# Performance work log

Measured on AMD Instinct MI355X. Metric: run time of the kernel, lower is better.

The kernel has to match this reference:

```python
import jax, jax.numpy as jnp
import numpy as np

B, T, HID = 1, 256, 2048
H, D = 16, 128
KD = H * D
CONV = 4
MAX_CG = 30
LAMB_LB = 0.25
NORM_EPS = 1e-5


def setup_inputs() -> dict:
    key = jax.random.key(0)
    ks = jax.random.split(key, 10)
    s = 0.02
    init_lamb = float(np.log(np.exp(1.0 - LAMB_LB) - 1.0))  # softplus^-1(1 - lower_bound)
    return {
        "hidden_states": jax.random.normal(ks[0], (B, T, HID), jnp.float32),
        "Wq": jax.random.normal(ks[1], (HID, KD), jnp.float32) * s,
        "Wk": jax.random.normal(ks[2], (HID, KD), jnp.float32) * s,
        "Wv": jax.random.normal(ks[3], (HID, KD), jnp.float32) * s,
        "Wa": jax.random.normal(ks[4], (HID, H), jnp.float32) * s,
        "ba": jnp.full((H,), 2.0, jnp.float32),
        "Wb": jax.random.normal(ks[5], (HID, H), jnp.float32) * s,
        "bb": jnp.zeros((H,), jnp.float32),
        "conv_wq": jax.random.normal(ks[6], (KD, CONV), jnp.float32) * s,
        "conv_wk": jax.random.normal(ks[7], (KD, CONV), jnp.float32) * s,
        "lambda_params": jnp.full((KD,), init_lamb, jnp.float32),
        "o_norm_w": jnp.ones((D,), jnp.float32),
        "Wo": jax.random.normal(ks[8], (KD, HID), jnp.float32) * s,
    }


def short_conv_silu(x, w):
    # depthwise causal conv over time; x [b,t,c], w [c,k]
    k = w.shape[1]
    xp = jnp.pad(x, ((0, 0), (k - 1, 0), (0, 0)))
    t = x.shape[1]
    y = xp[:, 0:t, :] * w[:, 0]
    for i in range(1, k):
        y = y + xp[:, i:i + t, :] * w[:, i]
    return jax.nn.silu(y)


def l2norm(x):
    return x * jax.lax.rsqrt(jnp.sum(x * x, -1, keepdims=True) + 1e-6)


def rmsnorm(x, w):
    return x * jax.lax.rsqrt(jnp.mean(x * x, -1, keepdims=True) + NORM_EPS) * w


def cg_solve(A, b):
    # solve A x = b per (batch, head) with fixed CG iterations, x0 = 0
    matvec = lambda p: jnp.einsum('bhij,bhj->bhi', A, p)
    x0 = jnp.zeros_like(b)
    rs0 = jnp.sum(b * b, -1)

    def body(i, st):
        xc, r, p, rs = st
        Ap = matvec(p)
        alpha = rs / (jnp.sum(p * Ap, -1) + 1e-12)
        xc = xc + alpha[..., None] * p
        r = r - alpha[..., None] * Ap
        rs_n = jnp.sum(r * r, -1)
        p = r + (rs_n / (rs + 1e-12))[..., None] * p
        return xc, r, p, rs_n

    xf, _, _, _ = jax.lax.fori_loop(0, MAX_CG, body, (x0, b, b, rs0))
    return xf


def mesa_recurrence(q, k, v, g, beta, lamb_diag):
    # q,k,v [b,t,h,d]; g,beta [b,t,h]; lamb_diag [h,d,d]
    def step(carry, inp):
        h_kk, h_kv = carry
        qt, kt, vt, gt, bt = inp
        decay = jnp.exp(gt)[..., None, None]
        b_ = bt[..., None, None]
        h_kk = h_kk * decay + b_ * (kt[..., :, None] * kt[..., None, :])
        h_kv = h_kv * decay + b_ * (kt[..., :, None] * vt[..., None, :])
        A = h_kk + lamb_diag[None]
        q_star = cg_solve(A, qt)
        ot = jnp.einsum('bhk,bhkv->bhv', q_star, h_kv)
        return (h_kk, h_kv), ot

    init = (jnp.zeros((B, H, D, D), q.dtype), jnp.zeros((B, H, D, D), q.dtype))
    xs = (q.transpose(1, 0, 2, 3), k.transpose(1, 0, 2, 3), v.transpose(1, 0, 2, 3),
          g.transpose(1, 0, 2), beta.transpose(1, 0, 2))
    _, o = jax.lax.scan(step, init, xs)
    return o.transpose(1, 0, 2, 3)  # [b,t,h,d]


def reference(hidden_states, Wq, Wk, Wv, Wa, ba, Wb, bb, conv_wq, conv_wk,
              lambda_params, o_norm_w, Wo):
    x = hidden_states
    q = short_conv_silu(x @ Wq, conv_wq)
    k = short_conv_silu(x @ Wk, conv_wk)
    v = x @ Wv
    q = l2norm(q.reshape(B, T, H, D))
    k = l2norm(k.reshape(B, T, H, D))
    v = v.reshape(B, T, H, D)
    beta = jax.nn.sigmoid(x @ Wb + bb)          # [b,t,h]
    g = jax.nn.log_sigmoid(x @ Wa + ba)          # [b,t,h]
    lamb = (jax.nn.softplus(lambda_params) + LAMB_LB).reshape(H, D)
    lamb_diag = lamb[:, :, None] * jnp.eye(D, dtype=lamb.dtype)  # [h,d,d]
    o = mesa_recurrence(q, k, v, g, beta, lamb_diag)
    o = rmsnorm(o, o_norm_w)
    o = o.reshape(B, T, KD) @ Wo
    return o
```

## Files before the change

kernel.cpp:

```cpp
#include <hip/hip_runtime.h>
#include <math.h>

#define TT 256
#define HIDDEN 2048
#define NH 16
#define HD 128
#define KDIM 2048
#define NCG 30

typedef _Float16 h2 __attribute__((ext_vector_type(2)));
typedef _Float16 h4 __attribute__((ext_vector_type(4)));
typedef _Float16 half8 __attribute__((ext_vector_type(8)));
typedef float floatx4 __attribute__((ext_vector_type(4)));

__device__ __forceinline__ float wave_sum64(float v) {
#pragma unroll
    for (int off = 32; off > 0; off >>= 1) v += __shfl_xor(v, off, 64);
    return v;
}

__device__ __forceinline__ half8 cvt8(const float4 x, const float4 y) {
    half8 f;
    f[0] = (_Float16)x.x; f[1] = (_Float16)x.y; f[2] = (_Float16)x.z; f[3] = (_Float16)x.w;
    f[4] = (_Float16)y.x; f[5] = (_Float16)y.y; f[6] = (_Float16)y.z; f[7] = (_Float16)y.w;
    return f;
}

__device__ __forceinline__ void glds16(const void* g, void* l) {
    __builtin_amdgcn_global_load_lds(
        (const __attribute__((address_space(1))) void*)g,
        (__attribute__((address_space(3))) void*)l, 16, 0, 0);
}

__global__ __launch_bounds__(256) void wtrans_kernel(
    const float* __restrict__ W0, const float* __restrict__ W1,
    const float* __restrict__ W2, const float* __restrict__ W3,
    _Float16* __restrict__ T0, _Float16* __restrict__ T1,
    _Float16* __restrict__ T2, _Float16* __restrict__ T3,
    const float* __restrict__ Wa, const float* __restrict__ Wb,
    _Float16* __restrict__ Tabb)
{
    __shared__ float tile[64][68];
    const int z = blockIdx.z;
    const int tid = threadIdx.x;
    int k0, n0;
    _Float16* __restrict__ T;

    if (z == 4) {
        const int y = blockIdx.y;
        if (y >= 2) return;
        k0 = blockIdx.x * 64; n0 = y * 64;
        T = Tabb;
#pragma unroll
        for (int p = 0; p < 4; p++) {
            const int idx = p * 256 + tid;
            const int r = idx >> 4, c = (idx & 15) * 4;
            float4 v = make_float4(0.f, 0.f, 0.f, 0.f);
            if (y == 0 && c < 32) {
                const float* src = (c < 16) ? &Wa[(size_t)(k0 + r) * NH + c]
                                            : &Wb[(size_t)(k0 + r) * NH + (c - 16)];
                v = *(const float4*)src;
            }
            tile[r][c] = v.x; tile[r][c + 1] = v.y; tile[r][c + 2] = v.z; tile[r][c + 3] = v.w;
        }
    } else {
        const float* __restrict__ W = (z == 0) ? W0 : (z == 1) ? W1 : (z == 2) ? W2 : W3;
        T = (z == 0) ? T0 : (z == 1) ? T1 : (z == 2) ? T2 : T3;
        k0 = blockIdx.x * 64; n0 = blockIdx.y * 64;
#pragma unroll
        for (int p = 0; p < 4; p++) {
            const int idx = p * 256 + tid;
            const int r = idx >> 4, c = (idx & 15) * 4;
            const float4 v = *(const float4*)&W[(size_t)(k0 + r) * KDIM + n0 + c];
            tile[r][c] = v.x; tile[r][c + 1] = v.y; tile[r][c + 2] = v.z; tile[r][c + 3] = v.w;
        }
    }
    __syncthreads();
#pragma unroll
    for (int p = 0; p < 2; p++) {
        const int slot = p * 256 + tid;
        const int ktc = slot >> 6, nn_loc = slot & 63;
        const int gk = k0 + ktc * 8, gn = n0 + nn_loc;
        const int nt = gn >> 7, nn = gn & 127;
        const int kt = gk >> 5, kc = (gk >> 3) & 3;
        half8 o;
#pragma unroll
        for (int j = 0; j < 8; j++) o[j] = (_Float16)tile[ktc * 8 + j][nn_loc];
        *(half8*)&T[(size_t)(((nt * 64 + kt) * 4 + kc)) * 1024 + nn * 8] = o;
    }
}

#define ASTR 72
__global__ __launch_bounds__(256) void gemm_kernel(
    const float* __restrict__ A,
    const _Float16* __restrict__ Bb0, const _Float16* __restrict__ Bb1,
    const _Float16* __restrict__ Bb2, const _Float16* __restrict__ Bb3,
    float* __restrict__ C0, float* __restrict__ C1, float* __restrict__ C2,
    const float* __restrict__ ba, const float* __restrict__ bb,
    float* __restrict__ g, float* __restrict__ beta)
{
    __shared__ __align__(16) _Float16 Bsh[2][8192];
    __shared__ __align__(16) _Float16 Ash[2][32 * ASTR];

    const int tid = threadIdx.x, lane = tid & 63, w = tid >> 6;
    const int q = lane >> 4, l16 = lane & 15;

    const int b = blockIdx.x;
    const int xcd = b & 7, gslot = b >> 3;
    int nt, mt;
    if (gslot < 48) { nt = xcd * 6 + (gslot >> 3); mt = gslot & 7; }
    else           { nt = 48;                      mt = xcd; }
    const int mat = nt >> 4;
    const int ntile = nt & 15;
    const int n0 = ntile * 128;
    const _Float16* __restrict__ Bb = (mat == 0) ? Bb0 : (mat == 1) ? Bb1 : (mat == 2) ? Bb2 : Bb3;
    float* __restrict__ C = (mat == 0) ? C0 : (mat == 1) ? C1 : C2;
    const int m0 = mt * 32;

    const _Float16* __restrict__ Btile = Bb + (size_t)ntile * 262144;
    const int ar = tid >> 3, ac = (tid & 7) * 8;
    const float* __restrict__ Ap = &A[(size_t)(m0 + ar) * KDIM + ac];

    floatx4 acc[2][2] = {};
    float4 ax, ay;

#pragma unroll
    for (int i = 0; i < 4; i++)
        glds16(Btile + (size_t)((w * 4 + i) * 64 + lane) * 8, &Bsh[0][(w * 4 + i) * 512]);
    ax = *(const float4*)&Ap[0]; ay = *(const float4*)&Ap[4];
    *(half8*)&Ash[0][ar * ASTR + ac] = cvt8(ax, ay);
    ax = *(const float4*)&Ap[64]; ay = *(const float4*)&Ap[68];
    __syncthreads();

    const int NSTEP = KDIM / 64;
    for (int s = 0; s < NSTEP; s++) {
        const int cur = s & 1;
        if (s + 1 < NSTEP) {
            const _Float16* src = Btile + (size_t)(s + 1) * 8192;
#pragma unroll
            for (int i = 0; i < 4; i++)
                glds16(src + (size_t)((w * 4 + i) * 64 + lane) * 8, &Bsh[cur ^ 1][(w * 4 + i) * 512]);
        }
#pragma unroll
        for (int kk = 0; kk < 2; kk++) {
            const half8 bf0 = *(const half8*)&Bsh[cur][kk * 4096 + q * 1024 + (w * 32 + l16) * 8];
            const half8 bf1 = *(const half8*)&Bsh[cur][kk * 4096 + q * 1024 + (w * 32 + 16 + l16) * 8];
            const half8 af0 = *(const half8*)&Ash[cur][l16 * ASTR + kk * 32 + q * 8];
            const half8 af1 = *(const half8*)&Ash[cur][(16 + l16) * ASTR + kk * 32 + q * 8];
            acc[0][0] = __builtin_amdgcn_mfma_f32_16x16x32_f16(af0, bf0, acc[0][0], 0, 0, 0);
            acc[0][1] = __builtin_amdgcn_mfma_f32_16x16x32_f16(af0, bf1, acc[0][1], 0, 0, 0);
            acc[1][0] = __builtin_amdgcn_mfma_f32_16x16x32_f16(af1, bf0, acc[1][0], 0, 0, 0);
            acc[1][1] = __builtin_amdgcn_mfma_f32_16x16x32_f16(af1, bf1, acc[1][1], 0, 0, 0);
        }
        if (s + 1 < NSTEP) {
            *(half8*)&Ash[cur ^ 1][ar * ASTR + ac] = cvt8(ax, ay);
            if (s + 2 < NSTEP) {
                ax = *(const float4*)&Ap[(s + 2) * 64];
                ay = *(const float4*)&Ap[(s + 2) * 64 + 4];
            }
        }
        __syncthreads();
    }

    if (mat == 3) {
        if (w == 0) {
            const float bav = ba[l16], bbv = bb[l16];
#pragma unroll
            for (int r = 0; r < 4; r++) {
                const int t0r = m0 + q * 4 + r, t1r = m0 + 16 + q * 4 + r;
                float z0 = acc[0][0][r] + bav;
                g[t0r * NH + l16] = fminf(z0, 0.f) - log1pf(__expf(-fabsf(z0)));
                float z1 = acc[0][1][r] + bbv;
                beta[t0r * NH + l16] = 1.f / (1.f + __expf(-z1));
                float z2 = acc[1][0][r] + bav;
                g[t1r * NH + l16] = fminf(z2, 0.f) - log1pf(__expf(-fabsf(z2)));
                float z3 = acc[1][1][r] + bbv;
                beta[t1r * NH + l16] = 1.f / (1.f + __expf(-z3));
            }
        }
        return;
    }

#pragma unroll
    for (int r = 0; r < 4; r++) {
        C[(size_t)(m0 + q * 4 + r) * KDIM + n0 + w * 32 + l16] = acc[0][0][r];
        C[(size_t)(m0 + q * 4 + r) * KDIM + n0 + w * 32 + 16 + l16] = acc[0][1][r];
        C[(size_t)(m0 + 16 + q * 4 + r) * KDIM + n0 + w * 32 + l16] = acc[1][0][r];
        C[(size_t)(m0 + 16 + q * 4 + r) * KDIM + n0 + w * 32 + 16 + l16] = acc[1][1][r];
    }
}

__global__ __launch_bounds__(256) void gemm64_kernel(
    const float* __restrict__ A, const _Float16* __restrict__ Bb,
    float* __restrict__ C)
{
    __shared__ __align__(16) _Float16 Bsh[2][4096];
    __shared__ __align__(16) _Float16 Ash[2][32 * ASTR];

    const int tid = threadIdx.x, lane = tid & 63, w = tid >> 6;
    const int q = lane >> 4, l16 = lane & 15;
    const int b = blockIdx.x;
    const int xcd = b & 7, gslot = b >> 3;
    const int nt = xcd * 4 + (gslot >> 3), mt = gslot & 7;
    const int n0 = nt * 64, m0 = mt * 32;
    const int nt128 = nt >> 1;
    const size_t nnoff = (size_t)(nt & 1) * 512;

    const _Float16* __restrict__ Btile = Bb + (size_t)nt128 * 262144;
    const int ar = tid >> 3, ac = (tid & 7) * 8;
    const float* __restrict__ Ap = &A[(size_t)(m0 + ar) * KDIM + ac];

    floatx4 acc0 = {}, acc1 = {};
    float4 ax, ay;

    const int c0 = w * 2, c1 = w * 2 + 1;
    auto bsrc = [&](int s, int chunk) {
        const int kt2 = chunk >> 2, kc = chunk & 3;
        return Btile + (size_t)((s * 2 + kt2) * 4 + kc) * 1024 + nnoff + (size_t)lane * 8;
    };

    glds16(bsrc(0, c0), &Bsh[0][c0 * 512]);
    glds16(bsrc(0, c1), &Bsh[0][c1 * 512]);
    ax = *(const float4*)&Ap[0]; ay = *(const float4*)&Ap[4];
    *(half8*)&Ash[0][ar * ASTR + ac] = cvt8(ax, ay);
    ax = *(const float4*)&Ap[64]; ay = *(const float4*)&Ap[68];
    __syncthreads();

    const int NSTEP = KDIM / 64;
    for (int s = 0; s < NSTEP; s++) {
        const int cur = s & 1;
        if (s + 1 < NSTEP) {
            glds16(bsrc(s + 1, c0), &Bsh[cur ^ 1][c0 * 512]);
            glds16(bsrc(s + 1, c1), &Bsh[cur ^ 1][c1 * 512]);
        }
#pragma unroll
        for (int kk = 0; kk < 2; kk++) {
            const half8 bf  = *(const half8*)&Bsh[cur][kk * 2048 + q * 512 + (w * 16 + l16) * 8];
            const half8 af0 = *(const half8*)&Ash[cur][l16 * ASTR + kk * 32 + q * 8];
            const half8 af1 = *(const half8*)&Ash[cur][(16 + l16) * ASTR + kk * 32 + q * 8];
            acc0 = __builtin_amdgcn_mfma_f32_16x16x32_f16(af0, bf, acc0, 0, 0, 0);
            acc1 = __builtin_amdgcn_mfma_f32_16x16x32_f16(af1, bf, acc1, 0, 0, 0);
        }
        if (s + 1 < NSTEP) {
            *(half8*)&Ash[cur ^ 1][ar * ASTR + ac] = cvt8(ax, ay);
            if (s + 2 < NSTEP) {
                ax = *(const float4*)&Ap[(s + 2) * 64];
                ay = *(const float4*)&Ap[(s + 2) * 64 + 4];
            }
        }
        __syncthreads();
    }

#pragma unroll
    for (int r = 0; r < 4; r++) {
        C[(size_t)(m0 + q * 4 + r) * KDIM + n0 + w * 16 + l16] = acc0[r];
        C[(size_t)(m0 + 16 + q * 4 + r) * KDIM + n0 + w * 16 + l16] = acc1[r];
    }
}

__global__ __launch_bounds__(256) void conv_silu_l2_kernel(
    const float* __restrict__ q_pre, const float* __restrict__ k_pre,
    const float* __restrict__ cwq, const float* __restrict__ cwk,
    float* __restrict__ qn, float* __restrict__ kn)
{
    const int t = blockIdx.x, h = blockIdx.y;
    const int which = threadIdx.x >> 7, d = threadIdx.x & 127;
    const int w = threadIdx.x >> 6;
    const int c = h * HD + d;
    const float* pre = which ? k_pre : q_pre;
    const float* cw  = which ? cwk : cwq;
    float y = 0.f;
#pragma unroll
    for (int i = 0; i < 4; i++) {
        const int ts = t - 3 + i;
        if (ts >= 0) y = fmaf(pre[ts * KDIM + c], cw[c * 4 + i], y);
    }
    const float s = y / (1.f + __expf(-y));
    float v = s * s;
#pragma unroll
    for (int off = 32; off > 0; off >>= 1) v += __shfl_down(v, off, 64);
    __shared__ float red[4];
    if ((threadIdx.x & 63) == 0) red[w] = v;
    __syncthreads();
    const float sum = red[which * 2] + red[which * 2 + 1];
    float* dst = which ? kn : qn;
    dst[t * KDIM + c] = s * rsqrtf(sum + 1e-6f);
}

#define PSTR 136
#define YSTR 264

template<int SMAX>
__device__ __forceinline__ void mesa_cg(
    const float* __restrict__ qn, const float* __restrict__ kn, const float* __restrict__ vv,
    const float* __restrict__ g, const float* __restrict__ bet, const float* __restrict__ lp,
    const float* __restrict__ onw, float* __restrict__ out,
    int h, int t0, _Float16* Psh, _Float16* Ysh, float* red,
    float* Gsh, float* bets)
{
    constexpr int NSUB1 = SMAX / 64;
    constexpr int NK2   = SMAX / 32;

    const int tid = threadIdx.x, lane = tid & 63, w = tid >> 6;
    const int quad = lane >> 4, l16 = lane & 15;
    const int tmy = t0 + l16;
    const int dbase = w * 32;

    {
        float sc = g[tid * NH + h];
#pragma unroll
        for (int off = 1; off < 64; off <<= 1) {
            const float o = __shfl_up(sc, off, 64);
            if (lane >= off) sc += o;
        }
        if (lane == 63) red[w] = sc;
        bets[tid] = bet[tid * NH + h];
        __syncthreads();
        float woff = 0.f;
        for (int u = 0; u < w; u++) woff += red[u];
        Gsh[tid] = sc + woff;
        __syncthreads();
    }

    half8 K1[NSUB1][4];
#pragma unroll
    for (int ii = 0; ii < NSUB1; ii++) {
        const int srow = 16 * (w + 4 * ii) + l16;
        const float* kp = &kn[(srow * NH + h) * HD];
#pragma unroll
        for (int kk = 0; kk < 4; kk++) {
            const float4 a = *(const float4*)&kp[kk * 32 + quad * 8];
            const float4 b = *(const float4*)&kp[kk * 32 + quad * 8 + 4];
            K1[ii][kk] = cvt8(a, b);
        }
    }

    half8 KtF[2][NK2];
#pragma unroll
    for (int ss = 0; ss < 2; ss++) {
        const int d = dbase + ss * 16 + l16;
#pragma unroll
        for (int kk = 0; kk < NK2; kk++) {
#pragma unroll
            for (int j = 0; j < 8; j++) {
                const int s = kk * 32 + quad * 8 + j;
                KtF[ss][kk][j] = (_Float16)kn[(s * NH + h) * HD + d];
            }
        }
    }

    half8 Vf[NK2][2];
#pragma unroll
    for (int kk = 0; kk < NK2; kk++) {
#pragma unroll
        for (int ss = 0; ss < 2; ss++) {
            const int dv = dbase + ss * 16 + l16;
#pragma unroll
            for (int j = 0; j < 8; j++) {
                const int s = kk * 32 + quad * 8 + j;
                Vf[kk][ss][j] = (_Float16)vv[(s * NH + h) * HD + dv];
            }
        }
    }

    const float Gt = Gsh[tmy];
    float Wm[NSUB1][4];
#pragma unroll
    for (int ii = 0; ii < NSUB1; ii++)
#pragma unroll
        for (int r = 0; r < 4; r++) {
            const int s = 16 * (w + 4 * ii) + quad * 4 + r;
            Wm[ii][r] = (s <= tmy) ? bets[s] * __expf(Gt - Gsh[s]) : 0.f;
        }
    float lam[8], xv[8], rv[8], pv[8];
#pragma unroll
    for (int ss = 0; ss < 2; ss++)
#pragma unroll
        for (int r = 0; r < 4; r++) {
            const int e = ss * 4 + r;
            const int d = dbase + ss * 16 + quad * 4 + r;
            const float lx = lp[h * HD + d];
            lam[e] = fmaxf(lx, 0.f) + log1pf(__expf(-fabsf(lx))) + 0.25f;
            const float b = qn[(tmy * NH + h) * HD + d];
            xv[e] = 0.f; rv[e] = b; pv[e] = b;
        }
    float rs = 0.f;
#pragma unroll
    for (int e = 0; e < 8; e++) rs += rv[e] * rv[e];
    rs += __shfl_xor(rs, 16, 64); rs += __shfl_xor(rs, 32, 64);

    auto writeP = [&](const float* src) {
#pragma unroll
        for (int ss = 0; ss < 2; ss++) {
            h4 ph;
            ph.x = (_Float16)src[ss * 4 + 0]; ph.y = (_Float16)src[ss * 4 + 1];
            ph.z = (_Float16)src[ss * 4 + 2]; ph.w = (_Float16)src[ss * 4 + 3];
            *(h4*)&Psh[l16 * PSTR + dbase + ss * 16 + quad * 4] = ph;
        }
    };
    writeP(pv);

    for (int it = 0; it <= NCG; it++) {
        __syncthreads();
        floatx4 acc1a[NSUB1] = {}, acc1b[NSUB1] = {};
#pragma unroll
        for (int kk = 0; kk < 2; kk++) {
            const half8 bfa = *(const half8*)&Psh[l16 * PSTR + kk * 32 + quad * 8];
            const half8 bfb = *(const half8*)&Psh[l16 * PSTR + (kk + 2) * 32 + quad * 8];
#pragma unroll
            for (int ii = 0; ii < NSUB1; ii++) {
                acc1a[ii] = __builtin_amdgcn_mfma_f32_16x16x32_f16(K1[ii][kk], bfa, acc1a[ii], 0, 0, 0);
                acc1b[ii] = __builtin_amdgcn_mfma_f32_16x16x32_f16(K1[ii][kk + 2], bfb, acc1b[ii], 0, 0, 0);
            }
        }
#pragma unroll
        for (int ii = 0; ii < NSUB1; ii++) {
            h4 yh;
            yh.x = (_Float16)(Wm[ii][0] * (acc1a[ii][0] + acc1b[ii][0]));
            yh.y = (_Float16)(Wm[ii][1] * (acc1a[ii][1] + acc1b[ii][1]));
            yh.z = (_Float16)(Wm[ii][2] * (acc1a[ii][2] + acc1b[ii][2]));
            yh.w = (_Float16)(Wm[ii][3] * (acc1a[ii][3] + acc1b[ii][3]));
            *(h4*)&Ysh[l16 * YSTR + 16 * (w + 4 * ii) + quad * 4] = yh;
        }
        __syncthreads();
        if (it == NCG) break;

        floatx4 acc2a[2] = {}, acc2b[2] = {};
#pragma unroll
        for (int kk = 0; kk < NK2; kk += 2) {
            const half8 bf0 = *(const half8*)&Ysh[l16 * YSTR + kk * 32 + quad * 8];
            const half8 bf1 = *(const half8*)&Ysh[l16 * YSTR + (kk + 1) * 32 + quad * 8];
#pragma unroll
            for (int ss = 0; ss < 2; ss++) {
                acc2a[ss] = __builtin_amdgcn_mfma_f32_16x16x32_f16(KtF[ss][kk], bf0, acc2a[ss], 0, 0, 0);
                acc2b[ss] = __builtin_amdgcn_mfma_f32_16x16x32_f16(KtF[ss][kk + 1], bf1, acc2b[ss], 0, 0, 0);
            }
        }
        float Ap[8], pAp = 0.f;
#pragma unroll
        for (int ss = 0; ss < 2; ss++)
#pragma unroll
            for (int r = 0; r < 4; r++) {
                const int e = ss * 4 + r;
                Ap[e] = (acc2a[ss][r] + acc2b[ss][r]) + lam[e] * pv[e];
                pAp = fmaf(pv[e], Ap[e], pAp);
            }
        pAp += __shfl_xor(pAp, 16, 64); pAp += __shfl_xor(pAp, 32, 64);
        const float alpha = rs / (pAp + 1e-12f);
        float rsn = 0.f;
#pragma unroll
        for (int e = 0; e < 8; e++) {
            xv[e] = fmaf(alpha, pv[e], xv[e]);
            rv[e] = fmaf(-alpha, Ap[e], rv[e]);
            rsn = fmaf(rv[e], rv[e], rsn);
        }
        rsn += __shfl_xor(rsn, 16, 64); rsn += __shfl_xor(rsn, 32, 64);
        const float bcg = rsn / (rs + 1e-12f);
#pragma unroll
        for (int e = 0; e < 8; e++) pv[e] = fmaf(bcg, pv[e], rv[e]);
        rs = rsn;
        writeP(it == NCG - 1 ? xv : pv);
    }

    floatx4 accOa[2] = {}, accOb[2] = {};
#pragma unroll
    for (int kk = 0; kk < NK2; kk += 2) {
        const half8 af0 = *(const half8*)&Ysh[l16 * YSTR + kk * 32 + quad * 8];
        const half8 af1 = *(const half8*)&Ysh[l16 * YSTR + (kk + 1) * 32 + quad * 8];
#pragma unroll
        for (int ss = 0; ss < 2; ss++) {
            accOa[ss] = __builtin_amdgcn_mfma_f32_16x16x32_f16(af0, Vf[kk][ss], accOa[ss], 0, 0, 0);
            accOb[ss] = __builtin_amdgcn_mfma_f32_16x16x32_f16(af1, Vf[kk + 1][ss], accOb[ss], 0, 0, 0);
        }
    }
    float accO[2][4];
#pragma unroll
    for (int ss = 0; ss < 2; ss++)
#pragma unroll
        for (int r = 0; r < 4; r++) accO[ss][r] = accOa[ss][r] + accOb[ss][r];

    float part[4];
#pragma unroll
    for (int r = 0; r < 4; r++) {
        part[r] = accO[0][r] * accO[0][r] + accO[1][r] * accO[1][r];
#pragma unroll
        for (int off = 1; off < 16; off <<= 1) part[r] += __shfl_xor(part[r], off, 64);
    }
    if (l16 == 0) {
#pragma unroll
        for (int r = 0; r < 4; r++) red[w * 16 + quad * 4 + r] = part[r];
    }
    __syncthreads();
    const float w0 = onw[dbase + l16], w1 = onw[dbase + 16 + l16];
#pragma unroll
    for (int r = 0; r < 4; r++) {
        const int qr = quad * 4 + r;
        const float sumd = red[qr] + red[16 + qr] + red[32 + qr] + red[48 + qr];
        const float sc = rsqrtf(sumd * (1.f / HD) + 1e-5f);
        const int trow = ((t0 + qr) * NH + h) * HD;
        out[trow + dbase + l16] = accO[0][r] * sc * w0;
        out[trow + dbase + 16 + l16] = accO[1][r] * sc * w1;
    }
}

__global__ __launch_bounds__(256, 1) void mesa_kernel(
    const float* __restrict__ qn, const float* __restrict__ kn, const float* __restrict__ vv,
    const float* __restrict__ g, const float* __restrict__ bet, const float* __restrict__ lp,
    const float* __restrict__ onw, float* __restrict__ out)
{
    __shared__ __align__(16) _Float16 Psh[16 * PSTR];
    __shared__ __align__(16) _Float16 Ysh[16 * YSTR];
    __shared__ float red[64];
    __shared__ float Gsh[256];
    __shared__ float bets[256];
    const int h = blockIdx.x, jb = blockIdx.y, t0 = jb * 16;
    switch (jb >> 2) {
        case 0:  mesa_cg<64> (qn, kn, vv, g, bet, lp, onw, out, h, t0, Psh, Ysh, red, Gsh, bets); break;
        case 1:  mesa_cg<128>(qn, kn, vv, g, bet, lp, onw, out, h, t0, Psh, Ysh, red, Gsh, bets); break;
        case 2:  mesa_cg<192>(qn, kn, vv, g, bet, lp, onw, out, h, t0, Psh, Ysh, red, Gsh, bets); break;
        default: mesa_cg<256>(qn, kn, vv, g, bet, lp, onw, out, h, t0, Psh, Ysh, red, Gsh, bets); break;
    }
}

extern "C" void kernel_launch(void* const* d_in, const int* in_sizes, int n_in,
                              void* d_out, int out_size, void* d_ws, size_t ws_size,
                              hipStream_t stream)
{
    (void)in_sizes; (void)n_in; (void)out_size; (void)ws_size;
    const float* x   = (const float*)d_in[0];
    const float* Wq  = (const float*)d_in[1];
    const float* Wk  = (const float*)d_in[2];
    const float* Wv  = (const float*)d_in[3];
    const float* Wa  = (const float*)d_in[4];
    const float* ba  = (const float*)d_in[5];
    const float* Wb  = (const float*)d_in[6];
    const float* bb  = (const float*)d_in[7];
    const float* cwq = (const float*)d_in[8];
    const float* cwk = (const float*)d_in[9];
    const float* lp  = (const float*)d_in[10];
    const float* onw = (const float*)d_in[11];
    const float* Wo  = (const float*)d_in[12];

    char* wsb = (char*)d_ws;
    float* q_pre = (float*)wsb;
    float* k_pre = q_pre + 524288;
    float* v     = k_pre + 524288;
    float* qn    = v + 524288;
    float* kn    = qn + 524288;
    float* g     = kn + 524288;
    float* beta  = g + 4096;
    float* G     = beta + 4096;
    float* lamb  = G + 4096;
    size_t off = ((size_t)((char*)(lamb + 2048) - wsb) + 1023) & ~(size_t)1023;
    _Float16* WtQ = (_Float16*)(wsb + off);
    _Float16* WtK = WtQ + (size_t)KDIM * KDIM;
    _Float16* WtV = WtK + (size_t)KDIM * KDIM;
    _Float16* WtO = WtV + (size_t)KDIM * KDIM;
    _Float16* Tabb = WtO + (size_t)KDIM * KDIM;
    float* onorm  = q_pre;
    float* outp   = (float*)d_out;

    wtrans_kernel<<<dim3(32, 32, 5), 256, 0, stream>>>(Wq, Wk, Wv, Wo, WtQ, WtK, WtV, WtO,
                                                       Wa, Wb, Tabb);

    gemm_kernel<<<dim3(392), 256, 0, stream>>>(x, WtQ, WtK, WtV, Tabb,
                                               q_pre, k_pre, v, ba, bb, g, beta);
    conv_silu_l2_kernel<<<dim3(TT, NH), 256, 0, stream>>>(q_pre, k_pre, cwq, cwk, qn, kn);

    mesa_kernel<<<dim3(NH, 16), 256, 0, stream>>>(qn, kn, v, g, beta, lp, onw, onorm);

    gemm64_kernel<<<dim3(256), 256, 0, stream>>>(onorm, WtO, outp);
}
```

Baseline: 226.9 us.

## Fuse weight fp16 conversion into GEMM loads, drop separate transpose kernel

Removes the standalone weight transpose/convert kernel and instead has each GEMM load fp32 weights directly from global memory into registers, convert them to fp16, and write them into the shared-memory B tile layout. The goal is to avoid a full extra pass that reads about 64 MB of fp32 weights and writes fp16 copies on every call. In exchange, each GEMM block now reads fp32 weights, twice the bytes of the fp16 copies, with strided per-lane scalar loads instead of async global-to-LDS loads. It also spends more registers on the prefetch buffers.

Result: faster. 222.4 us (-2.0%).

```diff
diff --git a/kernel.cpp b/kernel.cpp
--- a/kernel.cpp
+++ b/kernel.cpp
@@ -8,16 +8,9 @@
 #define KDIM 2048
 #define NCG 30
 
-typedef _Float16 h2 __attribute__((ext_vector_type(2)));
 typedef _Float16 h4 __attribute__((ext_vector_type(4)));
 typedef _Float16 half8 __attribute__((ext_vector_type(8)));
 typedef float floatx4 __attribute__((ext_vector_type(4)));
-
-__device__ __forceinline__ float wave_sum64(float v) {
-#pragma unroll
-    for (int off = 32; off > 0; off >>= 1) v += __shfl_xor(v, off, 64);
-    return v;
-}
 
 __device__ __forceinline__ half8 cvt8(const float4 x, const float4 y) {
     half8 f;
@@ -26,75 +19,12 @@
     return f;
 }
 
-__device__ __forceinline__ void glds16(const void* g, void* l) {
-    __builtin_amdgcn_global_load_lds(
-        (const __attribute__((address_space(1))) void*)g,
-        (__attribute__((address_space(3))) void*)l, 16, 0, 0);
-}
-
-__global__ __launch_bounds__(256) void wtrans_kernel(
-    const float* __restrict__ W0, const float* __restrict__ W1,
-    const float* __restrict__ W2, const float* __restrict__ W3,
-    _Float16* __restrict__ T0, _Float16* __restrict__ T1,
-    _Float16* __restrict__ T2, _Float16* __restrict__ T3,
-    const float* __restrict__ Wa, const float* __restrict__ Wb,
-    _Float16* __restrict__ Tabb)
-{
-    __shared__ float tile[64][68];
-    const int z = blockIdx.z;
-    const int tid = threadIdx.x;
-    int k0, n0;
-    _Float16* __restrict__ T;
-
-    if (z == 4) {
-        const int y = blockIdx.y;
-        if (y >= 2) return;
-        k0 = blockIdx.x * 64; n0 = y * 64;
-        T = Tabb;
-#pragma unroll
-        for (int p = 0; p < 4; p++) {
-            const int idx = p * 256 + tid;
-            const int r = idx >> 4, c = (idx & 15) * 4;
-            float4 v = make_float4(0.f, 0.f, 0.f, 0.f);
-            if (y == 0 && c < 32) {
-                const float* src = (c < 16) ? &Wa[(size_t)(k0 + r) * NH + c]
-                                            : &Wb[(size_t)(k0 + r) * NH + (c - 16)];
-                v = *(const float4*)src;
-            }
-            tile[r][c] = v.x; tile[r][c + 1] = v.y; tile[r][c + 2] = v.z; tile[r][c + 3] = v.w;
-        }
-    } else {
-        const float* __restrict__ W = (z == 0) ? W0 : (z == 1) ? W1 : (z == 2) ? W2 : W3;
-        T = (z == 0) ? T0 : (z == 1) ? T1 : (z == 2) ? T2 : T3;
-        k0 = blockIdx.x * 64; n0 = blockIdx.y * 64;
-#pragma unroll
-        for (int p = 0; p < 4; p++) {
-            const int idx = p * 256 + tid;
-            const int r = idx >> 4, c = (idx & 15) * 4;
-            const float4 v = *(const float4*)&W[(size_t)(k0 + r) * KDIM + n0 + c];
-            tile[r][c] = v.x; tile[r][c + 1] = v.y; tile[r][c + 2] = v.z; tile[r][c + 3] = v.w;
-        }
-    }
-    __syncthreads();
-#pragma unroll
-    for (int p = 0; p < 2; p++) {
-        const int slot = p * 256 + tid;
-        const int ktc = slot >> 6, nn_loc = slot & 63;
-        const int gk = k0 + ktc * 8, gn = n0 + nn_loc;
-        const int nt = gn >> 7, nn = gn & 127;
-        const int kt = gk >> 5, kc = (gk >> 3) & 3;
-        half8 o;
-#pragma unroll
-        for (int j = 0; j < 8; j++) o[j] = (_Float16)tile[ktc * 8 + j][nn_loc];
-        *(half8*)&T[(size_t)(((nt * 64 + kt) * 4 + kc)) * 1024 + nn * 8] = o;
-    }
-}
-
 #define ASTR 72
 __global__ __launch_bounds__(256) void gemm_kernel(
     const float* __restrict__ A,
-    const _Float16* __restrict__ Bb0, const _Float16* __restrict__ Bb1,
-    const _Float16* __restrict__ Bb2, const _Float16* __restrict__ Bb3,
+    const float* __restrict__ Wq, const float* __restrict__ Wk,
+    const float* __restrict__ Wv,
+    const float* __restrict__ Wa, const float* __restrict__ Wb,
     float* __restrict__ C0, float* __restrict__ C1, float* __restrict__ C2,
     const float* __restrict__ ba, const float* __restrict__ bb,
     float* __restrict__ g, float* __restrict__ beta)
@@ -113,20 +43,76 @@
     const int mat = nt >> 4;
     const int ntile = nt & 15;
     const int n0 = ntile * 128;
-    const _Float16* __restrict__ Bb = (mat == 0) ? Bb0 : (mat == 1) ? Bb1 : (mat == 2) ? Bb2 : Bb3;
+    const float* __restrict__ W = (mat == 0) ? Wq : (mat == 1) ? Wk : (mat == 2) ? Wv : Wa;
     float* __restrict__ C = (mat == 0) ? C0 : (mat == 1) ? C1 : C2;
     const int m0 = mt * 32;
-
-    const _Float16* __restrict__ Btile = Bb + (size_t)ntile * 262144;
+    const int kt2 = w >> 1;
+
     const int ar = tid >> 3, ac = (tid & 7) * 8;
     const float* __restrict__ Ap = &A[(size_t)(m0 + ar) * KDIM + ac];
 
     floatx4 acc[2][2] = {};
     float4 ax, ay;
-
-#pragma unroll
-    for (int i = 0; i < 4; i++)
-        glds16(Btile + (size_t)((w * 4 + i) * 64 + lane) * 8, &Bsh[0][(w * 4 + i) * 512]);
+    float bwv[2][16];
+    float bab[16];
+
+    auto loadB = [&](int s) {
+        const float* base = &W[(size_t)(s * 64 + w * 16) * KDIM + n0 + lane];
+#pragma unroll
+        for (int i = 0; i < 16; i++) {
+            bwv[0][i] = base[(size_t)i * KDIM];
+            bwv[1][i] = base[(size_t)i * KDIM + 64];
+        }
+    };
+    auto writeB = [&](int buf) {
+#pragma unroll
+        for (int hf = 0; hf < 2; hf++)
+#pragma unroll
+            for (int kg = 0; kg < 2; kg++) {
+                const int kc = (w * 2 + kg) & 3;
+                half8 h;
+#pragma unroll
+                for (int j = 0; j < 8; j++) h[j] = (_Float16)bwv[hf][kg * 8 + j];
+                *(half8*)&Bsh[buf][((kt2 * 4 + kc) * 128 + hf * 64 + lane) * 8] = h;
+            }
+    };
+    auto loadBab = [&](int s) {
+        if (w >= 2) return;
+        const float* __restrict__ Wsrc = (w == 0) ? Wa : Wb;
+        const int hh = lane & 15, ko = lane >> 4;
+#pragma unroll
+        for (int hf = 0; hf < 2; hf++)
+#pragma unroll
+            for (int j = 0; j < 8; j++)
+                bab[hf * 8 + j] = Wsrc[(size_t)(s * 64 + hf * 32 + ko * 8 + j) * NH + hh];
+    };
+    auto writeBab = [&](int buf) {
+        if (w >= 2) return;
+        const int hh = lane & 15, ko = lane >> 4;
+        const int nn = w * 16 + hh;
+#pragma unroll
+        for (int hf = 0; hf < 2; hf++) {
+            half8 h;
+#pragma unroll
+            for (int j = 0; j < 8; j++) h[j] = (_Float16)bab[hf * 8 + j];
+            *(half8*)&Bsh[buf][((hf * 4 + ko) * 128 + nn) * 8] = h;
+        }
+    };
+
+    if (mat == 3) {
+        half8 z = {};
+#pragma unroll
+        for (int i = 0; i < 6; i++) {
+            const int idx = i * 256 + tid;
+            const int buf = idx & 1;
+            const int rest = idx >> 1;
+            const int slot = rest / 96, nrel = rest - slot * 96;
+            *(half8*)&Bsh[buf][(slot * 128 + 32 + nrel) * 8] = z;
+        }
+        loadBab(0); writeBab(0); loadBab(1);
+    } else {
+        loadB(0); writeB(0); loadB(1);
+    }
     ax = *(const float4*)&Ap[0]; ay = *(const float4*)&Ap[4];
     *(half8*)&Ash[0][ar * ASTR + ac] = cvt8(ax, ay);
     ax = *(const float4*)&Ap[64]; ay = *(const float4*)&Ap[68];
@@ -135,12 +121,6 @@
     const int NSTEP = KDIM / 64;
     for (int s = 0; s < NSTEP; s++) {
         const int cur = s & 1;
-        if (s + 1 < NSTEP) {
-            const _Float16* src = Btile + (size_t)(s + 1) * 8192;
-#pragma unroll
-            for (int i = 0; i < 4; i++)
-                glds16(src + (size_t)((w * 4 + i) * 64 + lane) * 8, &Bsh[cur ^ 1][(w * 4 + i) * 512]);
-        }
 #pragma unroll
         for (int kk = 0; kk < 2; kk++) {
             const half8 bf0 = *(const half8*)&Bsh[cur][kk * 4096 + q * 1024 + (w * 32 + l16) * 8];
@@ -153,6 +133,13 @@
             acc[1][1] = __builtin_amdgcn_mfma_f32_16x16x32_f16(af1, bf1, acc[1][1], 0, 0, 0);
         }
         if (s + 1 < NSTEP) {
+            if (mat == 3) {
+                writeBab(cur ^ 1);
+                if (s + 2 < NSTEP) loadBab(s + 2);
+            } else {
+                writeB(cur ^ 1);
+                if (s + 2 < NSTEP) loadB(s + 2);
+            }
             *(half8*)&Ash[cur ^ 1][ar * ASTR + ac] = cvt8(ax, ay);
             if (s + 2 < NSTEP) {
                 ax = *(const float4*)&Ap[(s + 2) * 64];
@@ -191,7 +178,7 @@
 }
 
 __global__ __launch_bounds__(256) void gemm64_kernel(
-    const float* __restrict__ A, const _Float16* __restrict__ Bb,
+    const float* __restrict__ A, const float* __restrict__ Wo,
     float* __restrict__ C)
 {
     __shared__ __align__(16) _Float16 Bsh[2][4096];
@@ -203,24 +190,32 @@
     const int xcd = b & 7, gslot = b >> 3;
     const int nt = xcd * 4 + (gslot >> 3), mt = gslot & 7;
     const int n0 = nt * 64, m0 = mt * 32;
-    const int nt128 = nt >> 1;
-    const size_t nnoff = (size_t)(nt & 1) * 512;
-
-    const _Float16* __restrict__ Btile = Bb + (size_t)nt128 * 262144;
+    const int kt2 = w >> 1;
+
     const int ar = tid >> 3, ac = (tid & 7) * 8;
     const float* __restrict__ Ap = &A[(size_t)(m0 + ar) * KDIM + ac];
 
     floatx4 acc0 = {}, acc1 = {};
     float4 ax, ay;
-
-    const int c0 = w * 2, c1 = w * 2 + 1;
-    auto bsrc = [&](int s, int chunk) {
-        const int kt2 = chunk >> 2, kc = chunk & 3;
-        return Btile + (size_t)((s * 2 + kt2) * 4 + kc) * 1024 + nnoff + (size_t)lane * 8;
-    };
-
-    glds16(bsrc(0, c0), &Bsh[0][c0 * 512]);
-    glds16(bsrc(0, c1), &Bsh[0][c1 * 512]);
+    float bwv[16];
+
+    auto loadB = [&](int s) {
+        const float* base = &Wo[(size_t)(s * 64 + w * 16) * KDIM + n0 + lane];
+#pragma unroll
+        for (int i = 0; i < 16; i++) bwv[i] = base[(size_t)i * KDIM];
+    };
+    auto writeB = [&](int buf) {
+#pragma unroll
+        for (int kg = 0; kg < 2; kg++) {
+            const int kc = (w * 2 + kg) & 3;
+            half8 h;
+#pragma unroll
+            for (int j = 0; j < 8; j++) h[j] = (_Float16)bwv[kg * 8 + j];
+            *(half8*)&Bsh[buf][((kt2 * 4 + kc) * 64 + lane) * 8] = h;
+        }
+    };
+
+    loadB(0); writeB(0); loadB(1);
     ax = *(const float4*)&Ap[0]; ay = *(const float4*)&Ap[4];
     *(half8*)&Ash[0][ar * ASTR + ac] = cvt8(ax, ay);
     ax = *(const float4*)&Ap[64]; ay = *(const float4*)&Ap[68];
@@ -229,10 +224,6 @@
     const int NSTEP = KDIM / 64;
     for (int s = 0; s < NSTEP; s++) {
         const int cur = s & 1;
-        if (s + 1 < NSTEP) {
-            glds16(bsrc(s + 1, c0), &Bsh[cur ^ 1][c0 * 512]);
-            glds16(bsrc(s + 1, c1), &Bsh[cur ^ 1][c1 * 512]);
-        }
 #pragma unroll
         for (int kk = 0; kk < 2; kk++) {
             const half8 bf  = *(const half8*)&Bsh[cur][kk * 2048 + q * 512 + (w * 16 + l16) * 8];
@@ -242,6 +233,8 @@
             acc1 = __builtin_amdgcn_mfma_f32_16x16x32_f16(af1, bf, acc1, 0, 0, 0);
         }
         if (s + 1 < NSTEP) {
+            writeB(cur ^ 1);
+            if (s + 2 < NSTEP) loadB(s + 2);
             *(half8*)&Ash[cur ^ 1][ar * ASTR + ac] = cvt8(ax, ay);
             if (s + 2 < NSTEP) {
                 ax = *(const float4*)&Ap[(s + 2) * 64];
@@ -549,25 +542,14 @@
     float* kn    = qn + 524288;
     float* g     = kn + 524288;
     float* beta  = g + 4096;
-    float* G     = beta + 4096;
-    float* lamb  = G + 4096;
-    size_t off = ((size_t)((char*)(lamb + 2048) - wsb) + 1023) & ~(size_t)1023;
-    _Float16* WtQ = (_Float16*)(wsb + off);
-    _Float16* WtK = WtQ + (size_t)KDIM * KDIM;
-    _Float16* WtV = WtK + (size_t)KDIM * KDIM;
-    _Float16* WtO = WtV + (size_t)KDIM * KDIM;
-    _Float16* Tabb = WtO + (size_t)KDIM * KDIM;
-    float* onorm  = q_pre;
-    float* outp   = (float*)d_out;
-
-    wtrans_kernel<<<dim3(32, 32, 5), 256, 0, stream>>>(Wq, Wk, Wv, Wo, WtQ, WtK, WtV, WtO,
-                                                       Wa, Wb, Tabb);
-
-    gemm_kernel<<<dim3(392), 256, 0, stream>>>(x, WtQ, WtK, WtV, Tabb,
+    float* onorm = q_pre;
+    float* outp  = (float*)d_out;
+
+    gemm_kernel<<<dim3(392), 256, 0, stream>>>(x, Wq, Wk, Wv, Wa, Wb,
                                                q_pre, k_pre, v, ba, bb, g, beta);
     conv_silu_l2_kernel<<<dim3(TT, NH), 256, 0, stream>>>(q_pre, k_pre, cwq, cwk, qn, kn);
 
     mesa_kernel<<<dim3(NH, 16), 256, 0, stream>>>(qn, kn, v, g, beta, lp, onw, onorm);
 
-    gemm64_kernel<<<dim3(256), 256, 0, stream>>>(onorm, WtO, outp);
-}
+    gemm64_kernel<<<dim3(256), 256, 0, stream>>>(onorm, Wo, outp);
+}
```
